# Kernel tuning notes

Measured on AMD Instinct MI355X. Metric: run time of the kernel, lower is better.

## Reference

```python
import jax, jax.numpy as jnp
import numpy as np

N_NODES, N_EDGES, F_IN = 8192, 32768, 16
N_SUB, N_GRAPH = 512, 32
EDGE_DIM, HID = 5, 128
DIMS = [(16, 32), (32, 64), (64, 64)]  # (M_in, M_out) per NNConv layer


def _segment_mean(x, seg, n):
    s = jax.ops.segment_sum(x, seg, num_segments=n)
    c = jax.ops.segment_sum(jnp.ones((x.shape[0], 1), x.dtype), seg, num_segments=n)
    return s / jnp.maximum(c, 1.0)


def _nnconv(x, src, dst, eattr, W1, b1, W2, b2, root, bias):
    # edge MLP -> per-edge weight matrix theta: [E, M_in, M_out]
    h = jax.nn.relu(eattr @ W1 + b1)
    theta = (h @ W2 + b2).reshape(-1, x.shape[1], root.shape[1])
    msg = jnp.einsum('ei,eio->eo', x[src], theta)          # gather + per-edge matvec
    agg = jax.ops.segment_sum(msg, dst, num_segments=x.shape[0])  # scatter-add (aggr='add')
    return agg + x @ root + bias


def setup_inputs() -> dict:
    key = jax.random.key(0)
    ks = jax.random.split(key, 32)
    inp = {}
    inp['x'] = jax.random.normal(ks[0], (N_NODES, F_IN), jnp.float32)
    inp['edge_index'] = jax.random.randint(ks[1], (2, N_EDGES), 0, N_NODES)
    inp['edge_attr'] = jax.random.uniform(ks[2], (N_EDGES, EDGE_DIM), jnp.float32)
    inp['node_to_subgraph'] = jnp.sort(jax.random.randint(ks[3], (N_NODES,), 0, N_SUB))
    inp['subgraph_to_graph'] = jnp.sort(jax.random.randint(ks[4], (N_SUB,), 0, N_GRAPH))
    i = 5
    for l, (ci, co) in enumerate(DIMS):
        inp[f'W1_{l}'] = jax.random.normal(ks[i], (EDGE_DIM, HID), jnp.float32) * 0.1
        inp[f'b1_{l}'] = jnp.zeros((HID,), jnp.float32)
        inp[f'W2_{l}'] = jax.random.normal(ks[i + 1], (HID, ci * co), jnp.float32) * 0.05
        inp[f'b2_{l}'] = jnp.zeros((ci * co,), jnp.float32)
        inp[f'root_{l}'] = jax.random.normal(ks[i + 2], (ci, co), jnp.float32) * 0.1
        inp[f'bias_{l}'] = jnp.zeros((co,), jnp.float32)
        i += 3
    inp['fc1_w'] = jax.random.normal(ks[i], (64, 32), jnp.float32) * 0.1
    inp['fc1_b'] = jnp.zeros((32,), jnp.float32)
    inp['fc2_w'] = jax.random.normal(ks[i + 1], (32, 16), jnp.float32) * 0.1
    inp['fc2_b'] = jnp.zeros((16,), jnp.float32)
    inp['fc3_w'] = jax.random.normal(ks[i + 2], (16, 1), jnp.float32) * 0.1
    inp['fc3_b'] = jnp.zeros((1,), jnp.float32)
    return inp


def reference(x, edge_index, edge_attr, node_to_subgraph, subgraph_to_graph,
              W1_0, b1_0, W2_0, b2_0, root_0, bias_0,
              W1_1, b1_1, W2_1, b2_1, root_1, bias_1,
              W1_2, b1_2, W2_2, b2_2, root_2, bias_2,
              fc1_w, fc1_b, fc2_w, fc2_b, fc3_w, fc3_b):
    src, dst = edge_index[0], edge_index[1]
    layers = [(W1_0, b1_0, W2_0, b2_0, root_0, bias_0),
              (W1_1, b1_1, W2_1, b2_1, root_1, bias_1),
              (W1_2, b1_2, W2_2, b2_2, root_2, bias_2)]
    h = x
    for (W1, b1, W2, b2, root, bias) in layers:
        h = jax.nn.elu(_nnconv(h, src, dst, edge_attr, W1, b1, W2, b2, root, bias))
    h = _segment_mean(h, node_to_subgraph, N_SUB)      # global_mean_pool over subgraphs
    h = _segment_mean(h, subgraph_to_graph, N_GRAPH)   # global_mean_pool over graphs
    h = jax.nn.elu(h @ fc1_w + fc1_b)
    h = jax.nn.elu(h @ fc2_w + fc2_b)
    return (h @ fc3_w + fc3_b).reshape(-1)
```

## Files before the change

kernel.cpp:

```cpp
#include <hip/hip_runtime.h>

#define E_EDGES 32768
#define NN 8192
#define HID 128
#define KS 4

typedef _Float16 half8 __attribute__((ext_vector_type(8)));
typedef _Float16 half4 __attribute__((ext_vector_type(4)));
typedef float f32x4 __attribute__((ext_vector_type(4)));

__global__ void zero_init_k(int* __restrict__ hist, float* __restrict__ pools, int npool) {
  int t = blockIdx.x * 256 + threadIdx.x;
  if (t < NN) hist[t] = 0;
  if (t < npool) pools[t] = 0.f;
}

__global__ void hist_k(const int* __restrict__ dst, int* __restrict__ hist) {
  int e = blockIdx.x * 256 + threadIdx.x;
  if (e < E_EDGES) atomicAdd(&hist[dst[e]], 1);
}

__global__ void scan_k(const int* __restrict__ hist, int* __restrict__ roff, int* __restrict__ cursor) {
  __shared__ int ps[1024];
  int t = threadIdx.x;
  int loc[8]; int s = 0;
  int base = t * 8;
#pragma unroll
  for (int j = 0; j < 8; ++j) { loc[j] = s; s += hist[base + j]; }
  ps[t] = s;
  __syncthreads();
  for (int off = 1; off < 1024; off <<= 1) {
    int v = 0;
    if (t >= off) v = ps[t - off];
    __syncthreads();
    if (t >= off) ps[t] += v;
    __syncthreads();
  }
  int excl = (t == 0) ? 0 : ps[t - 1];
#pragma unroll
  for (int j = 0; j < 8; ++j) { int v = excl + loc[j]; roff[base + j] = v; cursor[base + j] = v; }
  if (t == 1023) roff[NN] = ps[1023];
}

__global__ void scatter_k(const int* __restrict__ dst, int* __restrict__ cursor, int* __restrict__ eidx) {
  int e = blockIdx.x * 256 + threadIdx.x;
  if (e < E_EDGES) { int p = atomicAdd(&cursor[dst[e]], 1); eidx[p] = e; }
}

template <int CI, int CO>
__global__ void prep_b_k(const float* __restrict__ W2, const float* __restrict__ b2,
                         _Float16* __restrict__ out) {
  constexpr int Kmain = 128 * CI;
  constexpr int SPLITK = 32 * CI;
  constexpr int TAILK = ((SPLITK + CI + 127) / 128) * 128;
  constexpr int Kpad = 3 * SPLITK + TAILK;
  int idx = blockIdx.x * 256 + threadIdx.x;
  if (idx >= Kpad * CO) return;
  int j = idx & 7;
  int n = (idx >> 3) & (CO - 1);
  int kg = idx >> (3 + (CO == 64 ? 6 : 5));
  int k = kg * 8 + j;
  float v = 0.f;
  if (k < Kmain) {
    int h = k / CI, i = k & (CI - 1);
    v = W2[(h * CI + i) * CO + n];
  } else if (k < Kmain + CI) {
    int tt = k - Kmain;
    v = b2[tt * CO + n];
  }
  out[idx] = (_Float16)v;
}

template <int CI, int CO>
__launch_bounds__(256, 2)
__global__ void msg_mfma_k(const float* __restrict__ xcur, const int* __restrict__ src,
                           const float* __restrict__ eattr, const float* __restrict__ W1,
                           const float* __restrict__ b1, const _Float16* __restrict__ Bsw,
                           float* __restrict__ msgbuf) {
  constexpr int ME = 256;
  constexpr int L2CI = (CI == 64) ? 6 : ((CI == 32) ? 5 : 4);
  constexpr int Kmain = 128 * CI;
  constexpr int SPLITK = 32 * CI;
  constexpr int TAILK = ((SPLITK + CI + 127) / 128) * 128;
  constexpr int XSTR = CI + 8;
  constexpr int FC = CO / 16;
  constexpr int C4 = CI / 4;
  constexpr int L2C4 = L2CI - 2;

  __shared__ _Float16 he_s[32 * ME];
  __shared__ _Float16 xs_s[ME * XSTR];
  __shared__ float ea_s[ME * 5];
  __shared__ float W1s[5 * 32];
  __shared__ float b1s[32];
  __shared__ int src_s[ME];

  int t = threadIdx.x;
  int e0 = blockIdx.x * ME;
  int y = blockIdx.y;
  int hbeg = y * 32;

  for (int j = t; j < ME * 5; j += 256) ea_s[j] = eattr[e0 * 5 + j];
  if (t < 5 * 32) W1s[t] = W1[(t >> 5) * HID + hbeg + (t & 31)];
  if (t < 32) b1s[t] = b1[hbeg + t];
  src_s[t] = src[e0 + t];
  __syncthreads();

  for (int j = t; j < 32 * ME; j += 256) {
    int hl = j / ME, e = j & (ME - 1);
    float v = b1s[hl];
#pragma unroll
    for (int d = 0; d < 5; ++d) v += ea_s[e * 5 + d] * W1s[d * 32 + hl];
    he_s[hl * ME + e] = (_Float16)fmaxf(v, 0.f);
  }
  for (int j = t; j < ME * C4; j += 256) {
    int e = j >> L2C4, i4 = j & (C4 - 1);
    float4 v = ((const float4*)xcur)[src_s[e] * C4 + i4];
    half4 hq = {(_Float16)v.x, (_Float16)v.y, (_Float16)v.z, (_Float16)v.w};
    *(half4*)&xs_s[e * XSTR + i4 * 4] = hq;
  }
  __syncthreads();

  int lane = t & 63;
  int w = t >> 6;
  int quad = lane >> 4, l15 = lane & 15;

  int cbeg = y * (SPLITK / 32);
  int cend = cbeg + ((y < 3) ? (SPLITK / 32) : (TAILK / 32));
  int nrounds = (cend - cbeg) >> 2;

  const half8* bsw8 = (const half8*)Bsw;
  int ib = quad * CO + l15;

  f32x4 acc[4][FC];
#pragma unroll
  for (int fr = 0; fr < 4; ++fr)
#pragma unroll
    for (int fc = 0; fc < FC; ++fc)
#pragma unroll
      for (int r = 0; r < 4; ++r) acc[fr][fc][r] = 0.f;

  half8 breg[4][FC];
#pragma unroll
  for (int j = 0; j < 4; ++j)
#pragma unroll
    for (int fc = 0; fc < FC; ++fc)
      breg[j][fc] = bsw8[(cbeg + j) * 4 * CO + ib + fc * 16];

  for (int r = 0; r < nrounds; ++r) {
#pragma unroll
    for (int j = 0; j < 4; ++j) {
      int c = cbeg + r * 4 + j;
      int kq = c * 32 + quad * 8;
      int i = kq & (CI - 1);
      int hr = (kq >> L2CI) - hbeg;
      half8 a[4];
#pragma unroll
      for (int fr = 0; fr < 4; ++fr) {
        int e = w * 64 + fr * 16 + l15;
        half8 xv = *(const half8*)&xs_s[e * XSTR + i];
        _Float16 hv = (_Float16)1.f;
        if (kq < Kmain) hv = he_s[hr * ME + e];
        a[fr] = xv * hv;
      }
#pragma unroll
      for (int fc = 0; fc < FC; ++fc) {
#pragma unroll
        for (int fr = 0; fr < 4; ++fr)
          acc[fr][fc] = __builtin_amdgcn_mfma_f32_16x16x32_f16(a[fr], breg[j][fc], acc[fr][fc], 0, 0, 0);
      }
      int cn = c + 4;
      if (cn >= cend) cn = cend - 1;
#pragma unroll
      for (int fc = 0; fc < FC; ++fc)
        breg[j][fc] = bsw8[cn * 4 * CO + ib + fc * 16];
    }
  }

  float* mb = msgbuf + ((size_t)y * E_EDGES + e0) * CO;
#pragma unroll
  for (int fr = 0; fr < 4; ++fr)
#pragma unroll
    for (int fc = 0; fc < FC; ++fc)
#pragma unroll
      for (int r = 0; r < 4; ++r) {
        int el = w * 64 + fr * 16 + quad * 4 + r;
        int o = fc * 16 + l15;
        mb[el * CO + o] = acc[fr][fc][r];
      }
}

template <int CI, int CO>
__global__ void gather_elu_k(const float* __restrict__ xcur, const float* __restrict__ root,
                             const float* __restrict__ bias, const float* __restrict__ msgbuf,
                             const int* __restrict__ roff, const int* __restrict__ eidx,
                             float* __restrict__ xnext) {
  constexpr int NB = 256 / CO;
  __shared__ float xs[NB * CI];
  int t = threadIdx.x;
  int n0 = blockIdx.x * NB;
  for (int j = t; j < NB * CI; j += 256) xs[j] = xcur[n0 * CI + j];
  __syncthreads();
  int nl = t / CO, o = t & (CO - 1);
  int n = n0 + nl;
  float a = bias[o];
#pragma unroll
  for (int i = 0; i < CI; ++i) a += xs[nl * CI + i] * root[i * CO + o];
  int j1 = roff[n + 1];
  for (int j = roff[n]; j < j1; ++j) {
    int e = eidx[j];
    float m = 0.f;
#pragma unroll
    for (int s = 0; s < KS; ++s) m += msgbuf[((size_t)s * E_EDGES + e) * CO + o];
    a += m;
  }
  xnext[n * CO + o] = a > 0.f ? a : expm1f(a);
}

__global__ void pool_sub_k(const float* __restrict__ x3, const int* __restrict__ n2s,
                           float* __restrict__ ssum, float* __restrict__ scnt) {
  int idx = blockIdx.x * 256 + threadIdx.x;
  int n = idx >> 6, o = idx & 63;
  int s = n2s[n];
  atomicAdd(&ssum[(s << 6) + o], x3[idx]);
  if (o == 0) atomicAdd(&scnt[s], 1.f);
}

__global__ void pool_graph_k(const float* __restrict__ ssum, const float* __restrict__ scnt,
                             const int* __restrict__ s2g, float* __restrict__ gsum,
                             float* __restrict__ gcnt) {
  int idx = blockIdx.x * 256 + threadIdx.x;
  int s = idx >> 6, o = idx & 63;
  int g = s2g[s];
  float v = ssum[idx] / fmaxf(scnt[s], 1.f);
  atomicAdd(&gsum[(g << 6) + o], v);
  if (o == 0) atomicAdd(&gcnt[g], 1.f);
}

__global__ void head_k(const float* __restrict__ gsum, const float* __restrict__ gcnt,
                       const float* __restrict__ w1, const float* __restrict__ b1,
                       const float* __restrict__ w2, const float* __restrict__ b2,
                       const float* __restrict__ w3, const float* __restrict__ b3,
                       float* __restrict__ out) {
  int g = blockIdx.x;
  int t = threadIdx.x;
  __shared__ float m[64], s1[32], s2[16];
  float c = fmaxf(gcnt[g], 1.f);
  m[t] = gsum[g * 64 + t] / c;
  __syncthreads();
  if (t < 32) {
    float a = b1[t];
    for (int i = 0; i < 64; ++i) a += m[i] * w1[i * 32 + t];
    s1[t] = a > 0.f ? a : expm1f(a);
  }
  __syncthreads();
  if (t < 16) {
    float a = b2[t];
    for (int i = 0; i < 32; ++i) a += s1[i] * w2[i * 16 + t];
    s2[t] = a > 0.f ? a : expm1f(a);
  }
  __syncthreads();
  if (t == 0) {
    float a = b3[0];
    for (int i = 0; i < 16; ++i) a += s2[i] * w3[i];
    out[g] = a;
  }
}

extern "C" void kernel_launch(void* const* d_in, const int* in_sizes, int n_in,
                              void* d_out, int out_size, void* d_ws, size_t ws_size,
                              hipStream_t stream) {
  (void)in_sizes; (void)n_in; (void)out_size; (void)ws_size;
  const float* x0 = (const float*)d_in[0];
  const int* ei = (const int*)d_in[1];
  const float* ea = (const float*)d_in[2];
  const int* n2s = (const int*)d_in[3];
  const int* s2g = (const int*)d_in[4];
  const float* W1_[3] = {(const float*)d_in[5], (const float*)d_in[11], (const float*)d_in[17]};
  const float* b1_[3] = {(const float*)d_in[6], (const float*)d_in[12], (const float*)d_in[18]};
  const float* W2_[3] = {(const float*)d_in[7], (const float*)d_in[13], (const float*)d_in[19]};
  const float* b2_[3] = {(const float*)d_in[8], (const float*)d_in[14], (const float*)d_in[20]};
  const float* rt_[3] = {(const float*)d_in[9], (const float*)d_in[15], (const float*)d_in[21]};
  const float* bs_[3] = {(const float*)d_in[10], (const float*)d_in[16], (const float*)d_in[22]};
  const float* fc1w = (const float*)d_in[23]; const float* fc1b = (const float*)d_in[24];
  const float* fc2w = (const float*)d_in[25]; const float* fc2b = (const float*)d_in[26];
  const float* fc3w = (const float*)d_in[27]; const float* fc3b = (const float*)d_in[28];
  float* out = (float*)d_out;

  const int* srcp = ei;
  const int* dstp = ei + E_EDGES;

  char* wsb = (char*)d_ws;
  size_t off = 0;
  auto alloc = [&](size_t bytes) {
    void* p = wsb + off;
    off += (bytes + 255) & ~(size_t)255;
    return p;
  };
  _Float16* Bsw0 = (_Float16*)alloc((size_t)2176 * 32 * 2);
  _Float16* Bsw1 = (_Float16*)alloc((size_t)4224 * 64 * 2);
  _Float16* Bsw2 = (_Float16*)alloc((size_t)8320 * 64 * 2);
  float* msgbuf = (float*)alloc((size_t)KS * E_EDGES * 64 * 4);
  float* x1 = (float*)alloc((size_t)NN * 32 * 4);
  float* x2 = (float*)alloc((size_t)NN * 64 * 4);
  float* x3 = (float*)alloc((size_t)NN * 64 * 4);
  int* hist = (int*)alloc((size_t)NN * 4);
  int* roff = (int*)alloc((size_t)(NN + 1) * 4);
  int* cursor = (int*)alloc((size_t)NN * 4);
  int* eidx = (int*)alloc((size_t)E_EDGES * 4);
  const int npool = 512 * 64 + 512 + 32 * 64 + 32;
  float* pools = (float*)alloc((size_t)npool * 4);
  float* ssum = pools;
  float* scnt = pools + 512 * 64;
  float* gsum = scnt + 512;
  float* gcnt = gsum + 32 * 64;

  zero_init_k<<<(npool + 255) / 256, 256, 0, stream>>>(hist, pools, npool);
  hist_k<<<E_EDGES / 256, 256, 0, stream>>>(dstp, hist);
  scan_k<<<1, 1024, 0, stream>>>(hist, roff, cursor);
  scatter_k<<<E_EDGES / 256, 256, 0, stream>>>(dstp, cursor, eidx);
  prep_b_k<16, 32><<<(2176 * 32 + 255) / 256, 256, 0, stream>>>(W2_[0], b2_[0], Bsw0);
  prep_b_k<32, 64><<<(4224 * 64 + 255) / 256, 256, 0, stream>>>(W2_[1], b2_[1], Bsw1);
  prep_b_k<64, 64><<<(8320 * 64 + 255) / 256, 256, 0, stream>>>(W2_[2], b2_[2], Bsw2);

  dim3 mg(E_EDGES / 256, KS);
  msg_mfma_k<16, 32><<<mg, 256, 0, stream>>>(x0, srcp, ea, W1_[0], b1_[0], Bsw0, msgbuf);
  gather_elu_k<16, 32><<<NN / 8, 256, 0, stream>>>(x0, rt_[0], bs_[0], msgbuf, roff, eidx, x1);
  msg_mfma_k<32, 64><<<mg, 256, 0, stream>>>(x1, srcp, ea, W1_[1], b1_[1], Bsw1, msgbuf);
  gather_elu_k<32, 64><<<NN / 4, 256, 0, stream>>>(x1, rt_[1], bs_[1], msgbuf, roff, eidx, x2);
  msg_mfma_k<64, 64><<<mg, 256, 0, stream>>>(x2, srcp, ea, W1_[2], b1_[2], Bsw2, msgbuf);
  gather_elu_k<64, 64><<<NN / 4, 256, 0, stream>>>(x2, rt_[2], bs_[2], msgbuf, roff, eidx, x3);

  pool_sub_k<<<NN * 64 / 256, 256, 0, stream>>>(x3, n2s, ssum, scnt);
  pool_graph_k<<<512 * 64 / 256, 256, 0, stream>>>(ssum, scnt, s2g, gsum, gcnt);
  head_k<<<32, 64, 0, stream>>>(gsum, gcnt, fc1w, fc1b, fc2w, fc2b, fc3w, fc3b, out);
}
```

Measured before the change: 276.2 us.

## Fuse prep and pooling kernels, restructure MFMA A-operand loads with hoisted x fragments

Merges the three B-prep launches into one kernel. It folds subgraph pooling into the last gather kernel via atomics and combines graph pooling with the MLP head. In the message MFMA kernel, the edge-hidden buffer is transposed to edge-major with padding and x fragments are hoisted into registers once. The hidden scalars are then fetched per round rather than per k-chunk, and the bias tail is handled as a separate epilogue. This cuts launch count and LDS traffic in the hot loop, at the cost of more register pressure and more complex index logic.

```diff
diff --git a/kernel.cpp b/kernel.cpp
--- a/kernel.cpp
+++ b/kernel.cpp
@@ -48,14 +48,9 @@
 }
 
 template <int CI, int CO>
-__global__ void prep_b_k(const float* __restrict__ W2, const float* __restrict__ b2,
-                         _Float16* __restrict__ out) {
+__device__ inline void prep_b_one(int idx, const float* __restrict__ W2,
+                                  const float* __restrict__ b2, _Float16* __restrict__ out) {
   constexpr int Kmain = 128 * CI;
-  constexpr int SPLITK = 32 * CI;
-  constexpr int TAILK = ((SPLITK + CI + 127) / 128) * 128;
-  constexpr int Kpad = 3 * SPLITK + TAILK;
-  int idx = blockIdx.x * 256 + threadIdx.x;
-  if (idx >= Kpad * CO) return;
   int j = idx & 7;
   int n = (idx >> 3) & (CO - 1);
   int kg = idx >> (3 + (CO == 64 ? 6 : 5));
@@ -71,6 +66,18 @@
   out[idx] = (_Float16)v;
 }
 
+__global__ void prep_b_all_k(const float* __restrict__ W2_0, const float* __restrict__ b2_0, _Float16* __restrict__ o0,
+                             const float* __restrict__ W2_1, const float* __restrict__ b2_1, _Float16* __restrict__ o1,
+                             const float* __restrict__ W2_2, const float* __restrict__ b2_2, _Float16* __restrict__ o2) {
+  constexpr int N0 = 2176 * 32;
+  constexpr int N1 = 4224 * 64;
+  constexpr int N2 = 8320 * 64;
+  int idx = blockIdx.x * 256 + threadIdx.x;
+  if (idx < N0) prep_b_one<16, 32>(idx, W2_0, b2_0, o0);
+  else if (idx < N0 + N1) prep_b_one<32, 64>(idx - N0, W2_1, b2_1, o1);
+  else if (idx < N0 + N1 + N2) prep_b_one<64, 64>(idx - N0 - N1, W2_2, b2_2, o2);
+}
+
 template <int CI, int CO>
 __launch_bounds__(256, 2)
 __global__ void msg_mfma_k(const float* __restrict__ xcur, const int* __restrict__ src,
@@ -79,15 +86,15 @@
                            float* __restrict__ msgbuf) {
   constexpr int ME = 256;
   constexpr int L2CI = (CI == 64) ? 6 : ((CI == 32) ? 5 : 4);
-  constexpr int Kmain = 128 * CI;
-  constexpr int SPLITK = 32 * CI;
-  constexpr int TAILK = ((SPLITK + CI + 127) / 128) * 128;
   constexpr int XSTR = CI + 8;
+  constexpr int HSTR = 40;
   constexpr int FC = CO / 16;
   constexpr int C4 = CI / 4;
   constexpr int L2C4 = L2CI - 2;
-
-  __shared__ _Float16 he_s[32 * ME];
+  constexpr int NMAIN = CI / 4;
+  constexpr int XPN = (CI == 64) ? 2 : 1;
+
+  __shared__ _Float16 he_s[ME * HSTR];
   __shared__ _Float16 xs_s[ME * XSTR];
   __shared__ float ea_s[ME * 5];
   __shared__ float W1s[5 * 32];
@@ -106,11 +113,11 @@
   __syncthreads();
 
   for (int j = t; j < 32 * ME; j += 256) {
-    int hl = j / ME, e = j & (ME - 1);
+    int hl = j >> 8, e = j & 255;
     float v = b1s[hl];
 #pragma unroll
     for (int d = 0; d < 5; ++d) v += ea_s[e * 5 + d] * W1s[d * 32 + hl];
-    he_s[hl * ME + e] = (_Float16)fmaxf(v, 0.f);
+    he_s[e * HSTR + hl] = (_Float16)fmaxf(v, 0.f);
   }
   for (int j = t; j < ME * C4; j += 256) {
     int e = j >> L2C4, i4 = j & (C4 - 1);
@@ -123,14 +130,25 @@
   int lane = t & 63;
   int w = t >> 6;
   int quad = lane >> 4, l15 = lane & 15;
-
-  int cbeg = y * (SPLITK / 32);
-  int cend = cbeg + ((y < 3) ? (SPLITK / 32) : (TAILK / 32));
-  int nrounds = (cend - cbeg) >> 2;
+  int qsh = (quad >> 1) << 4;
+
+  int cbeg = y * CI;
+  int cend = cbeg + CI + ((y == 3) ? 4 : 0);
 
   const half8* bsw8 = (const half8*)Bsw;
   int ib = quad * CO + l15;
 
+  half8 xp[4][XPN];
+  const _Float16* hbp[4];
+#pragma unroll
+  for (int fr = 0; fr < 4; ++fr) {
+    int e = w * 64 + fr * 16 + l15;
+    int i0 = (CI == 16) ? ((quad & 1) * 8) : (quad * 8);
+    xp[fr][0] = *(const half8*)&xs_s[e * XSTR + i0];
+    if constexpr (CI == 64) xp[fr][1] = *(const half8*)&xs_s[e * XSTR + i0 + 32];
+    hbp[fr] = he_s + e * HSTR;
+  }
+
   f32x4 acc[4][FC];
 #pragma unroll
   for (int fr = 0; fr < 4; ++fr)
@@ -146,21 +164,36 @@
     for (int fc = 0; fc < FC; ++fc)
       breg[j][fc] = bsw8[(cbeg + j) * 4 * CO + ib + fc * 16];
 
-  for (int r = 0; r < nrounds; ++r) {
+  for (int r = 0; r < NMAIN; ++r) {
+    int c0 = cbeg + r * 4;
+    unsigned int hp2[4];
+    half4 hp4[4];
+    if constexpr (CI == 64) {
+      int oh = (c0 >> 1) - hbeg;
+#pragma unroll
+      for (int fr = 0; fr < 4; ++fr) hp2[fr] = *(const unsigned int*)(hbp[fr] + oh);
+    } else if constexpr (CI == 32) {
+      int oh = c0 - hbeg;
+#pragma unroll
+      for (int fr = 0; fr < 4; ++fr) hp4[fr] = *(const half4*)(hbp[fr] + oh);
+    }
 #pragma unroll
     for (int j = 0; j < 4; ++j) {
-      int c = cbeg + r * 4 + j;
-      int kq = c * 32 + quad * 8;
-      int i = kq & (CI - 1);
-      int hr = (kq >> L2CI) - hbeg;
+      int c = c0 + j;
       half8 a[4];
 #pragma unroll
       for (int fr = 0; fr < 4; ++fr) {
-        int e = w * 64 + fr * 16 + l15;
-        half8 xv = *(const half8*)&xs_s[e * XSTR + i];
-        _Float16 hv = (_Float16)1.f;
-        if (kq < Kmain) hv = he_s[hr * ME + e];
-        a[fr] = xv * hv;
+        if constexpr (CI == 64) {
+          unsigned short hb = (unsigned short)((j >= 2) ? (hp2[fr] >> 16) : hp2[fr]);
+          _Float16 hv = __builtin_bit_cast(_Float16, hb);
+          a[fr] = xp[fr][j & 1] * hv;
+        } else if constexpr (CI == 32) {
+          a[fr] = xp[fr][0] * hp4[fr][j];
+        } else {
+          unsigned int hw = *(const unsigned int*)(hbp[fr] + (2 * c - hbeg));
+          _Float16 hv = __builtin_bit_cast(_Float16, (unsigned short)(hw >> qsh));
+          a[fr] = xp[fr][0] * hv;
+        }
       }
 #pragma unroll
       for (int fc = 0; fc < FC; ++fc) {
@@ -176,6 +209,21 @@
     }
   }
 
+  if (y == 3) {
+#pragma unroll
+    for (int j = 0; j < 4; ++j) {
+      half8 a[4];
+#pragma unroll
+      for (int fr = 0; fr < 4; ++fr) a[fr] = xp[fr][(CI == 64) ? (j & 1) : 0];
+#pragma unroll
+      for (int fc = 0; fc < FC; ++fc) {
+#pragma unroll
+        for (int fr = 0; fr < 4; ++fr)
+          acc[fr][fc] = __builtin_amdgcn_mfma_f32_16x16x32_f16(a[fr], breg[j][fc], acc[fr][fc], 0, 0, 0);
+      }
+    }
+  }
+
   float* mb = msgbuf + ((size_t)y * E_EDGES + e0) * CO;
 #pragma unroll
   for (int fr = 0; fr < 4; ++fr)
@@ -189,11 +237,12 @@
       }
 }
 
-template <int CI, int CO>
+template <int CI, int CO, bool POOL>
 __global__ void gather_elu_k(const float* __restrict__ xcur, const float* __restrict__ root,
                              const float* __restrict__ bias, const float* __restrict__ msgbuf,
                              const int* __restrict__ roff, const int* __restrict__ eidx,
-                             float* __restrict__ xnext) {
+                             float* __restrict__ xnext, const int* __restrict__ n2s,
+                             float* __restrict__ ssum, float* __restrict__ scnt) {
   constexpr int NB = 256 / CO;
   __shared__ float xs[NB * CI];
   int t = threadIdx.x;
@@ -213,55 +262,52 @@
     for (int s = 0; s < KS; ++s) m += msgbuf[((size_t)s * E_EDGES + e) * CO + o];
     a += m;
   }
-  xnext[n * CO + o] = a > 0.f ? a : expm1f(a);
-}
-
-__global__ void pool_sub_k(const float* __restrict__ x3, const int* __restrict__ n2s,
-                           float* __restrict__ ssum, float* __restrict__ scnt) {
-  int idx = blockIdx.x * 256 + threadIdx.x;
-  int n = idx >> 6, o = idx & 63;
-  int s = n2s[n];
-  atomicAdd(&ssum[(s << 6) + o], x3[idx]);
-  if (o == 0) atomicAdd(&scnt[s], 1.f);
-}
-
-__global__ void pool_graph_k(const float* __restrict__ ssum, const float* __restrict__ scnt,
-                             const int* __restrict__ s2g, float* __restrict__ gsum,
-                             float* __restrict__ gcnt) {
-  int idx = blockIdx.x * 256 + threadIdx.x;
-  int s = idx >> 6, o = idx & 63;
-  int g = s2g[s];
-  float v = ssum[idx] / fmaxf(scnt[s], 1.f);
-  atomicAdd(&gsum[(g << 6) + o], v);
-  if (o == 0) atomicAdd(&gcnt[g], 1.f);
-}
-
-__global__ void head_k(const float* __restrict__ gsum, const float* __restrict__ gcnt,
-                       const float* __restrict__ w1, const float* __restrict__ b1,
-                       const float* __restrict__ w2, const float* __restrict__ b2,
-                       const float* __restrict__ w3, const float* __restrict__ b3,
-                       float* __restrict__ out) {
+  float v = a > 0.f ? a : expm1f(a);
+  if constexpr (POOL) {
+    int s = n2s[n];
+    atomicAdd(&ssum[(s << 6) + o], v);
+    if (o == 0) atomicAdd(&scnt[s], 1.f);
+  } else {
+    xnext[n * CO + o] = v;
+  }
+}
+
+__global__ void pg_head_k(const float* __restrict__ ssum, const float* __restrict__ scnt,
+                          const int* __restrict__ s2g,
+                          const float* __restrict__ w1, const float* __restrict__ b1,
+                          const float* __restrict__ w2, const float* __restrict__ b2,
+                          const float* __restrict__ w3, const float* __restrict__ b3,
+                          float* __restrict__ out) {
   int g = blockIdx.x;
   int t = threadIdx.x;
-  __shared__ float m[64], s1[32], s2[16];
-  float c = fmaxf(gcnt[g], 1.f);
-  m[t] = gsum[g * 64 + t] / c;
+  __shared__ int s2s[512];
+  __shared__ float hm[64], h1[32], h2[16];
+  for (int i = t; i < 512; i += 64) s2s[i] = s2g[i];
+  __syncthreads();
+  float acc = 0.f, cnt = 0.f;
+  for (int s = 0; s < 512; ++s) {
+    if (s2s[s] == g) {
+      acc += ssum[(s << 6) + t] / fmaxf(scnt[s], 1.f);
+      cnt += 1.f;
+    }
+  }
+  hm[t] = acc / fmaxf(cnt, 1.f);
   __syncthreads();
   if (t < 32) {
     float a = b1[t];
-    for (int i = 0; i < 64; ++i) a += m[i] * w1[i * 32 + t];
-    s1[t] = a > 0.f ? a : expm1f(a);
+    for (int i = 0; i < 64; ++i) a += hm[i] * w1[i * 32 + t];
+    h1[t] = a > 0.f ? a : expm1f(a);
   }
   __syncthreads();
   if (t < 16) {
     float a = b2[t];
-    for (int i = 0; i < 32; ++i) a += s1[i] * w2[i * 16 + t];
-    s2[t] = a > 0.f ? a : expm1f(a);
+    for (int i = 0; i < 32; ++i) a += h1[i] * w2[i * 16 + t];
+    h2[t] = a > 0.f ? a : expm1f(a);
   }
   __syncthreads();
   if (t == 0) {
     float a = b3[0];
-    for (int i = 0; i < 16; ++i) a += s2[i] * w3[i];
+    for (int i = 0; i < 16; ++i) a += h2[i] * w3[i];
     out[g] = a;
   }
 }
@@ -302,35 +348,29 @@
   float* msgbuf = (float*)alloc((size_t)KS * E_EDGES * 64 * 4);
   float* x1 = (float*)alloc((size_t)NN * 32 * 4);
   float* x2 = (float*)alloc((size_t)NN * 64 * 4);
-  float* x3 = (float*)alloc((size_t)NN * 64 * 4);
   int* hist = (int*)alloc((size_t)NN * 4);
   int* roff = (int*)alloc((size_t)(NN + 1) * 4);
   int* cursor = (int*)alloc((size_t)NN * 4);
   int* eidx = (int*)alloc((size_t)E_EDGES * 4);
-  const int npool = 512 * 64 + 512 + 32 * 64 + 32;
+  const int npool = 512 * 64 + 512;
   float* pools = (float*)alloc((size_t)npool * 4);
   float* ssum = pools;
   float* scnt = pools + 512 * 64;
-  float* gsum = scnt + 512;
-  float* gcnt = gsum + 32 * 64;
 
   zero_init_k<<<(npool + 255) / 256, 256, 0, stream>>>(hist, pools, npool);
   hist_k<<<E_EDGES / 256, 256, 0, stream>>>(dstp, hist);
   scan_k<<<1, 1024, 0, stream>>>(hist, roff, cursor);
   scatter_k<<<E_EDGES / 256, 256, 0, stream>>>(dstp, cursor, eidx);
-  prep_b_k<16, 32><<<(2176 * 32 + 255) / 256, 256, 0, stream>>>(W2_[0], b2_[0], Bsw0);
-  prep_b_k<32, 64><<<(4224 * 64 + 255) / 256, 256, 0, stream>>>(W2_[1], b2_[1], Bsw1);
-  prep_b_k<64, 64><<<(8320 * 64 + 255) / 256, 256, 0, stream>>>(W2_[2], b2_[2], Bsw2);
+  prep_b_all_k<<<(2176 * 32 + 4224 * 64 + 8320 * 64) / 256, 256, 0, stream>>>(
+      W2_[0], b2_[0], Bsw0, W2_[1], b2_[1], Bsw1, W2_[2], b2_[2], Bsw2);
 
   dim3 mg(E_EDGES / 256, KS);
   msg_mfma_k<16, 32><<<mg, 256, 0, stream>>>(x0, srcp, ea, W1_[0], b1_[0], Bsw0, msgbuf);
-  gather_elu_k<16, 32><<<NN / 8, 256, 0, stream>>>(x0, rt_[0], bs_[0], msgbuf, roff, eidx, x1);
+  gather_elu_k<16, 32, false><<<NN / 8, 256, 0, stream>>>(x0, rt_[0], bs_[0], msgbuf, roff, eidx, x1, nullptr, nullptr, nullptr);
   msg_mfma_k<32, 64><<<mg, 256, 0, stream>>>(x1, srcp, ea, W1_[1], b1_[1], Bsw1, msgbuf);
-  gather_elu_k<32, 64><<<NN / 4, 256, 0, stream>>>(x1, rt_[1], bs_[1], msgbuf, roff, eidx, x2);
+  gather_elu_k<32, 64, false><<<NN / 4, 256, 0, stream>>>(x1, rt_[1], bs_[1], msgbuf, roff, eidx, x2, nullptr, nullptr, nullptr);
   msg_mfma_k<64, 64><<<mg, 256, 0, stream>>>(x2, srcp, ea, W1_[2], b1_[2], Bsw2, msgbuf);
-  gather_elu_k<64, 64><<<NN / 4, 256, 0, stream>>>(x2, rt_[2], bs_[2], msgbuf, roff, eidx, x3);
-
-  pool_sub_k<<<NN * 64 / 256, 256, 0, stream>>>(x3, n2s, ssum, scnt);
-  pool_graph_k<<<512 * 64 / 256, 256, 0, stream>>>(ssum, scnt, s2g, gsum, gcnt);
-  head_k<<<32, 64, 0, stream>>>(gsum, gcnt, fc1w, fc1b, fc2w, fc2b, fc3w, fc3b, out);
-}
+  gather_elu_k<64, 64, true><<<NN / 4, 256, 0, stream>>>(x2, rt_[2], bs_[2], msgbuf, roff, eidx, nullptr, n2s, ssum, scnt);
+
+  pg_head_k<<<32, 64, 0, stream>>>(ssum, scnt, s2g, fc1w, fc1b, fc2w, fc2b, fc3w, fc3b, out);
+}
```

Result: slower. 286.5 us (+3.7%).
